# Performance work log

Measured on AMD Instinct MI355X. Metric: run time of the kernel, lower is better.

Reference implementation:

```python
import jax, jax.numpy as jnp
import numpy as np

N = 100000          # nodes
E = 1600000         # edges (before self-loops)
F_IN = 512          # num_node_features
H1, C1 = 8, 8       # layer-1 heads, per-head channels
NUM_CLASSES = 40
NEG_SLOPE = 0.2     # PyG GATConv default


def setup_inputs() -> dict:
    key = jax.random.key(0)
    ks = jax.random.split(key, 10)
    x = jax.random.normal(ks[0], (N, F_IN), jnp.float32)
    edge_index = jax.random.randint(ks[1], (2, E), 0, N, dtype=jnp.int64)
    # Glorot-ish scaled params (matches PyG init scale qualitatively)
    W1 = jax.random.normal(ks[2], (F_IN, H1 * C1), jnp.float32) / np.sqrt(F_IN)
    a_src1 = jax.random.normal(ks[3], (H1, C1), jnp.float32) / np.sqrt(C1)
    a_dst1 = jax.random.normal(ks[4], (H1, C1), jnp.float32) / np.sqrt(C1)
    b1 = jnp.zeros((H1 * C1,), jnp.float32)
    W2 = jax.random.normal(ks[5], (H1 * C1, NUM_CLASSES), jnp.float32) / np.sqrt(H1 * C1)
    a_src2 = jax.random.normal(ks[6], (1, NUM_CLASSES), jnp.float32) / np.sqrt(NUM_CLASSES)
    a_dst2 = jax.random.normal(ks[7], (1, NUM_CLASSES), jnp.float32) / np.sqrt(NUM_CLASSES)
    b2 = jnp.zeros((NUM_CLASSES,), jnp.float32)
    return {"x": x, "edge_index": edge_index, "W1": W1, "a_src1": a_src1,
            "a_dst1": a_dst1, "b1": b1, "W2": W2, "a_src2": a_src2,
            "a_dst2": a_dst2, "b2": b2}


def gat_layer(x, src, dst, W, a_s, a_d, b, concat):
    """PyG GATConv (eval mode: dropout=0). src -> dst messages, softmax over dst."""
    heads, ch = a_s.shape
    n = x.shape[0]
    h = (x @ W).reshape(n, heads, ch)                      # [N,H,C]
    alpha_s = jnp.einsum('nhc,hc->nh', h, a_s)             # [N,H]
    alpha_d = jnp.einsum('nhc,hc->nh', h, a_d)
    e = jax.nn.leaky_relu(alpha_s[src] + alpha_d[dst], NEG_SLOPE)   # [E,H]
    # segment softmax over incoming edges of each dst node
    m = jax.ops.segment_max(e, dst, num_segments=n)        # [N,H]
    p = jnp.exp(e - m[dst])
    s = jax.ops.segment_sum(p, dst, num_segments=n)
    alpha = p / (s[dst] + 1e-16)                           # [E,H]
    out = jax.ops.segment_sum(h[src] * alpha[..., None], dst, num_segments=n)  # [N,H,C]
    out = out.reshape(n, heads * ch) if concat else out.mean(axis=1)
    return out + b


def reference(x, edge_index, W1, a_src1, a_dst1, b1, W2, a_src2, a_dst2, b2):
    n = x.shape[0]
    loops = jnp.arange(n, dtype=edge_index.dtype)
    src = jnp.concatenate([edge_index[0], loops])          # add self-loops (PyG default)
    dst = jnp.concatenate([edge_index[1], loops])
    h = gat_layer(x, src, dst, W1, a_src1, a_dst1, b1, concat=True)
    h = jax.nn.elu(h)
    out = gat_layer(h, src, dst, W2, a_src2, a_dst2, b2, concat=False)
    return jax.nn.log_softmax(out, axis=1)
```

## Files before the change

### kernel.cpp

```cpp
#include <hip/hip_runtime.h>
#include <hip/hip_bf16.h>
#include <hip/hip_fp16.h>

#define F_IN 512
#define HC1 64
#define NH1 8
#define NC 40
#define NEG_SLOPE 0.2f
#define SCAN_CHUNK 2048
#define RADIX_EPB 4096
#define MAXNB 512
#define BCAP 8192

typedef short bf16x8 __attribute__((ext_vector_type(8)));
typedef float f32x4 __attribute__((ext_vector_type(4)));

static __device__ __forceinline__ unsigned short f2b(float f) {
    __hip_bfloat16 h = __float2bfloat16(f);
    return *(unsigned short*)&h;
}
static __device__ __forceinline__ float b2f(unsigned short u) {
    union { unsigned int i; float f; } v;
    v.i = ((unsigned int)u) << 16;
    return v.f;
}
static __device__ __forceinline__ unsigned short f2h(float f) {
    __half h = __float2half(f);
    return *(unsigned short*)&h;
}

__global__ void detect_i64(const int* __restrict__ ei, int* __restrict__ flag, int n_check) {
    __shared__ int found;
    if (threadIdx.x == 0) found = 0;
    __syncthreads();
    for (int i = threadIdx.x; i < n_check; i += 256) {
        if (ei[2 * i + 1] != 0) atomicOr(&found, 1);
    }
    __syncthreads();
    if (threadIdx.x == 0) *flag = (found == 0) ? 1 : 0;
}

__global__ void prep(const float* __restrict__ W1, const float* __restrict__ W2,
                     const float* __restrict__ a_s2, const float* __restrict__ a_d2,
                     unsigned short* __restrict__ wst, float* __restrict__ ws2,
                     float* __restrict__ wd2) {
    int t = blockIdx.x * 256 + threadIdx.x;
    if (t < 4096) {
        int p  = t & 7;
        int n  = (t >> 3) & 63;
        int kb = t >> 9;
        int l  = p ^ (n & 7);
        int k0 = kb * 64 + l * 8;
        unsigned short v[8];
#pragma unroll
        for (int j = 0; j < 8; j++) v[j] = f2b(W1[(size_t)(k0 + j) * HC1 + n]);
        *(uint4*)(wst + ((size_t)(kb * 64 + n) * 64 + p * 8)) = *(uint4*)v;
    }
    if (blockIdx.x == 0 && threadIdx.x < HC1) {
        int c = threadIdx.x;
        float s = 0.f, d = 0.f;
#pragma unroll
        for (int j = 0; j < NC; j++) {
            float w = W2[c * NC + j];
            s += w * a_s2[j];
            d += w * a_d2[j];
        }
        ws2[c] = s;
        wd2[c] = d;
    }
}

__global__ __launch_bounds__(256) void scatter1(const int* __restrict__ ei, const int* __restrict__ flag,
                                                int* __restrict__ deg, int* __restrict__ bcnt,
                                                int2* __restrict__ bpairs, int E, int NB) {
    __shared__ int cnt[MAXNB];
    __shared__ int gb[MAXNB];
    int tid = threadIdx.x;
    for (int i = tid; i < NB; i += 256) cnt[i] = 0;
    __syncthreads();
    int f = *flag;
    int base = blockIdx.x * RADIX_EPB;
    int sv[16], dv[16], rv[16];
#pragma unroll
    for (int i = 0; i < 16; i++) {
        int e = base + i * 256 + tid;
        if (e < E) {
            int s, d;
            if (f) { s = ei[2 * e]; d = ei[2 * (E + e)]; }
            else   { s = ei[e];     d = ei[E + e]; }
            sv[i] = s; dv[i] = d;
            rv[i] = atomicAdd(&cnt[d >> 8], 1);
            atomicAdd(&deg[d], 1);
        }
    }
    __syncthreads();
    for (int i = tid; i < NB; i += 256) {
        int c = cnt[i];
        gb[i] = c ? atomicAdd(&bcnt[i], c) : 0;
    }
    __syncthreads();
#pragma unroll
    for (int i = 0; i < 16; i++) {
        int e = base + i * 256 + tid;
        if (e < E) {
            int pos = gb[dv[i] >> 8] + rv[i];
            if (pos < BCAP)
                bpairs[(size_t)(dv[i] >> 8) * BCAP + pos] = make_int2(sv[i], dv[i]);
        }
    }
}

__global__ __launch_bounds__(256) void scan1(const int* __restrict__ deg, int* __restrict__ rowptr,
                                             int* __restrict__ bsums, int n) {
    __shared__ int sbuf[256];
    int tid = threadIdx.x;
    int base = blockIdx.x * SCAN_CHUNK + tid * 8;
    int v[8];
#pragma unroll
    for (int j = 0; j < 8; j++) { int idx = base + j; v[j] = (idx < n) ? deg[idx] : 0; }
    int tsum = 0;
#pragma unroll
    for (int j = 0; j < 8; j++) tsum += v[j];
    sbuf[tid] = tsum;
    __syncthreads();
    for (int off = 1; off < 256; off <<= 1) {
        int t = (tid >= off) ? sbuf[tid - off] : 0;
        __syncthreads();
        sbuf[tid] += t;
        __syncthreads();
    }
    int run = sbuf[tid] - tsum;
#pragma unroll
    for (int j = 0; j < 8; j++) {
        run += v[j];
        int idx = base + j;
        if (idx < n) rowptr[1 + idx] = run;
    }
    if (tid == 255) bsums[blockIdx.x] = sbuf[255];
}

__global__ __launch_bounds__(256) void scan23(int* __restrict__ rowptr,
                                              const int* __restrict__ bsums, int n, int nb) {
    __shared__ int soff[64];
    int tid = threadIdx.x;
    if (tid < 64) {
        int lane = tid;
        int v = (lane < nb) ? bsums[lane] : 0;
        int orig = v;
        for (int off = 1; off < 64; off <<= 1) {
            int t = __shfl_up(v, (unsigned)off, 64);
            if (lane >= off) v += t;
        }
        soff[lane] = v - orig;
    }
    __syncthreads();
    int i = blockIdx.x * 256 + tid;
    if (i < n) {
        rowptr[1 + i] += soff[i >> 11];
        if (i == 0) rowptr[0] = 0;
    }
}

__global__ __launch_bounds__(256) void scatter2(const int2* __restrict__ bpairs,
                                                const int* __restrict__ bcnt,
                                                const int* __restrict__ rowptr,
                                                int* __restrict__ col, int Nn) {
    __shared__ int cur[256];
    int b = blockIdx.x;
    int node0 = b << 8;
    int tid = threadIdx.x;
    int nlast = min(node0 + 256, Nn);
    if (node0 + tid < nlast) cur[tid] = rowptr[node0 + tid];
    __syncthreads();
    int cnt = min(bcnt[b], BCAP);
    const int2* bp = bpairs + (size_t)b * BCAP;
    for (int j = tid; j < cnt; j += 256) {
        int2 pr = bp[j];
        int pos = atomicAdd(&cur[pr.y - node0], 1);
        col[pos] = pr.x;
    }
}

__global__ __launch_bounds__(256) void gemm1(const float* __restrict__ x,
                                             const unsigned short* __restrict__ wst,
                                             const float* __restrict__ a_s, const float* __restrict__ a_d,
                                             unsigned short* __restrict__ h1, float* __restrict__ as1,
                                             float* __restrict__ ad1, int Nn) {
    __shared__ __align__(16) unsigned short smem[8192];
    unsigned short* xs = smem;
    unsigned short* ws = smem + 4096;
    int tid = threadIdx.x;
    int m0 = blockIdx.x * 64;
    int w = tid >> 6, lane = tid & 63;
    int quad = lane >> 4, mr = lane & 15;
    f32x4 acc[4];
#pragma unroll
    for (int i = 0; i < 4; i++) acc[i] = (f32x4){0.f, 0.f, 0.f, 0.f};

    int srow = tid >> 2;
    int sseg = tid & 3;
    bool rok = (m0 + srow) < Nn;
    const float* xrow = x + (size_t)(m0 + srow) * F_IN + sseg * 16;
    int swzw = (srow & 7) << 4;
    int swzr = (mr & 7) << 4;

    for (int kb = 0; kb < 8; kb++) {
        float4 xv0, xv1, xv2, xv3;
        if (rok) {
            const float4* xp = (const float4*)(xrow + kb * 64);
            xv0 = xp[0]; xv1 = xp[1]; xv2 = xp[2]; xv3 = xp[3];
        } else {
            xv0 = xv1 = xv2 = xv3 = make_float4(0.f, 0.f, 0.f, 0.f);
        }
        const uint4* wp = (const uint4*)(wst + (size_t)kb * 4096);
        uint4 wv0 = wp[tid];
        uint4 wv1 = wp[tid + 256];
        __syncthreads();
        {
            unsigned short bx[16];
            bx[0]  = f2b(xv0.x); bx[1]  = f2b(xv0.y); bx[2]  = f2b(xv0.z); bx[3]  = f2b(xv0.w);
            bx[4]  = f2b(xv1.x); bx[5]  = f2b(xv1.y); bx[6]  = f2b(xv1.z); bx[7]  = f2b(xv1.w);
            bx[8]  = f2b(xv2.x); bx[9]  = f2b(xv2.y); bx[10] = f2b(xv2.z); bx[11] = f2b(xv2.w);
            bx[12] = f2b(xv3.x); bx[13] = f2b(xv3.y); bx[14] = f2b(xv3.z); bx[15] = f2b(xv3.w);
            unsigned short* xr = xs + srow * 64;
            *(uint4*)(xr + ((((sseg * 32)      ) ^ swzw) >> 1)) = *(uint4*)&bx[0];
            *(uint4*)(xr + ((((sseg * 32) + 16 ) ^ swzw) >> 1)) = *(uint4*)&bx[8];
            ((uint4*)ws)[tid]       = wv0;
            ((uint4*)ws)[tid + 256] = wv1;
        }
        __syncthreads();
#pragma unroll
        for (int ks = 0; ks < 2; ks++) {
            int kc = ks * 64 + quad * 16;
            int co = (kc ^ swzr) >> 1;
            bf16x8 a = *(const bf16x8*)(xs + (w * 16 + mr) * 64 + co);
#pragma unroll
            for (int nb = 0; nb < 4; nb++) {
                bf16x8 b = *(const bf16x8*)(ws + (nb * 16 + mr) * 64 + co);
                acc[nb] = __builtin_amdgcn_mfma_f32_16x16x32_bf16(a, b, acc[nb], 0, 0, 0);
            }
        }
    }
    __syncthreads();
    unsigned short (*hs)[72] = (unsigned short(*)[72])smem;
#pragma unroll
    for (int nb = 0; nb < 4; nb++)
#pragma unroll
        for (int r = 0; r < 4; r++)
            hs[w * 16 + quad * 4 + r][nb * 16 + mr] = f2b(acc[nb][r]);
    __syncthreads();
    {
        if (rok) {
            uint4 v0 = *(const uint4*)&hs[srow][sseg * 16];
            uint4 v1 = *(const uint4*)&hs[srow][sseg * 16 + 8];
            uint4* dst = (uint4*)(h1 + (size_t)(m0 + srow) * HC1 + sseg * 16);
            dst[0] = v0;
            dst[1] = v1;
        }
    }
    for (int i = tid; i < 512; i += 256) {
        int row = i >> 3, hh = i & 7;
        if (m0 + row < Nn) {
            float s = 0.f, d = 0.f;
#pragma unroll
            for (int c = 0; c < 8; c++) {
                float v = b2f(hs[row][hh * 8 + c]);
                s += v * a_s[hh * 8 + c];
                d += v * a_d[hh * 8 + c];
            }
            as1[(size_t)(m0 + row) * NH1 + hh] = s;
            ad1[(size_t)(m0 + row) * NH1 + hh] = d;
        }
    }
}

__device__ __forceinline__ float lrelu(float e) { return e > 0.f ? e : NEG_SLOPE * e; }

__global__ __launch_bounds__(256) void agg1(const unsigned short* __restrict__ h1,
                                            const float* __restrict__ as1,
                                            const float* __restrict__ ad1, const int* __restrict__ rowptr,
                                            const int* __restrict__ col, const float* __restrict__ b1,
                                            const float* __restrict__ ws2, const float* __restrict__ wd2,
                                            unsigned short* __restrict__ h2b, float* __restrict__ as2,
                                            float* __restrict__ ad2, int Nn) {
    __shared__ float pbuf[4][NH1 * 68];
    int w = threadIdx.x >> 6;
    int wave = (blockIdx.x * 256 + threadIdx.x) >> 6;
    int lane = threadIdx.x & 63;
    if (wave >= Nn) return;
    int d = wave;
    int jb = rowptr[d], je = rowptr[d + 1];
    int half = lane >> 5;
    int cl = lane & 31;
    int head = cl >> 2;
    const float4* as4 = (const float4*)as1;
    const float4* ad4 = (const float4*)ad1;

    float4 dd0 = ad4[d * 2], dd1 = ad4[d * 2 + 1];
    float adh[8] = {dd0.x, dd0.y, dd0.z, dd0.w, dd1.x, dd1.y, dd1.z, dd1.w};
    float4 sd0 = as4[d * 2], sd1 = as4[d * 2 + 1];
    float svh[8] = {sd0.x, sd0.y, sd0.z, sd0.w, sd1.x, sd1.y, sd1.z, sd1.w};
    float e0[8];
#pragma unroll
    for (int h = 0; h < NH1; h++) e0[h] = lrelu(svh[h] + adh[h]);

    float acc0, acc1, ss;
    {
        unsigned gv = *(const unsigned*)(h1 + (size_t)d * HC1 + 2 * cl);
        union { unsigned i; float f; } lo, hi;
        lo.i = gv << 16; hi.i = gv & 0xffff0000u;
        if (half == 0) { acc0 = lo.f; acc1 = hi.f; ss = 1.f; }
        else           { acc0 = 0.f;  acc1 = 0.f;  ss = 0.f; }
    }
    float* pb = pbuf[w];

    for (int c0 = jb; c0 < je; c0 += 64) {
        int nc = min(64, je - c0);
        int srcv = d;
        if (lane < nc) {
            unsigned u = (unsigned)col[c0 + lane];
            srcv = (u < (unsigned)Nn) ? (int)u : d;
            float4 a0 = as4[srcv * 2], a1 = as4[srcv * 2 + 1];
            float ev[8] = {a0.x, a0.y, a0.z, a0.w, a1.x, a1.y, a1.z, a1.w};
#pragma unroll
            for (int h = 0; h < NH1; h++)
                pb[h * 68 + lane] = __expf(lrelu(ev[h] + adh[h]) - e0[h]);
        } else {
#pragma unroll
            for (int h = 0; h < NH1; h++) pb[h * 68 + lane] = 0.f;
        }
        int ncp = (nc + 7) & ~7;
        for (int jj = 0; jj < ncp; jj += 8) {
#pragma unroll
            for (int u4 = 0; u4 < 4; u4++) {
                int idx = jj + 2 * u4 + half;
                int s = __shfl(srcv, idx, 64);
                float p = pb[head * 68 + idx];
                unsigned gv = *(const unsigned*)(h1 + (size_t)s * HC1 + 2 * cl);
                union { unsigned i; float f; } lo, hi;
                lo.i = gv << 16; hi.i = gv & 0xffff0000u;
                acc0 += p * lo.f;
                acc1 += p * hi.f;
                ss += p;
            }
        }
    }
    acc0 += __shfl_xor(acc0, 32, 64);
    acc1 += __shfl_xor(acc1, 32, 64);
    ss   += __shfl_xor(ss, 32, 64);
    float inv = 1.f / (ss + 1e-16f);
    float o0 = acc0 * inv + b1[2 * cl];
    float o1 = acc1 * inv + b1[2 * cl + 1];
    o0 = o0 > 0.f ? o0 : __expf(o0) - 1.0f;
    o1 = o1 > 0.f ? o1 : __expf(o1) - 1.0f;
    if (half == 0) {
        unsigned pk = (unsigned)f2h(o0) | ((unsigned)f2h(o1) << 16);
        *(unsigned*)(h2b + (size_t)d * HC1 + 2 * cl) = pk;
    }
    float va = o0 * ws2[2 * cl] + o1 * ws2[2 * cl + 1];
    float vd = o0 * wd2[2 * cl] + o1 * wd2[2 * cl + 1];
#pragma unroll
    for (int off = 16; off; off >>= 1) {
        va += __shfl_xor(va, off, 64);
        vd += __shfl_xor(vd, off, 64);
    }
    if (lane == 0) { as2[d] = va; ad2[d] = vd; }
}

__global__ __launch_bounds__(256) void agg2(const unsigned short* __restrict__ h2b,
                                            const float* __restrict__ as2,
                                            const float* __restrict__ ad2, const int* __restrict__ rowptr,
                                            const int* __restrict__ col, const float* __restrict__ W2,
                                            const float* __restrict__ b2,
                                            float* __restrict__ out, int Nn) {
    __shared__ float pbuf[4][64];
    __shared__ float smv[4][64];
    __shared__ float W2s[HC1 * NC];
    int tid = threadIdx.x;
    for (int i = tid; i < HC1 * NC; i += 256) W2s[i] = W2[i];
    __syncthreads();
    int w = tid >> 6;
    int wave = (blockIdx.x * 256 + tid) >> 6;
    int lane = tid & 63;
    if (wave >= Nn) return;
    int d = wave;
    int jb = rowptr[d], je = rowptr[d + 1];
    int half = lane >> 5;
    int cl = lane & 31;
    float adv = ad2[d];
    float e0 = lrelu(as2[d] + adv);
    float acc0, acc1, ss;
    {
        unsigned gv = *(const unsigned*)(h2b + (size_t)d * HC1 + 2 * cl);
        union { unsigned u; __half2 h; } cv; cv.u = gv;
        float2 ff = __half22float2(cv.h);
        if (half == 0) { acc0 = ff.x; acc1 = ff.y; ss = 1.f; }
        else           { acc0 = 0.f;  acc1 = 0.f;  ss = 0.f; }
    }
    float* pb = pbuf[w];

    for (int c0 = jb; c0 < je; c0 += 64) {
        int nc = min(64, je - c0);
        int srcv = d;
        if (lane < nc) {
            unsigned u = (unsigned)col[c0 + lane];
            srcv = (u < (unsigned)Nn) ? (int)u : d;
            pb[lane] = __expf(lrelu(as2[srcv] + adv) - e0);
        } else {
            pb[lane] = 0.f;
        }
        int ncp = (nc + 7) & ~7;
        for (int jj = 0; jj < ncp; jj += 8) {
#pragma unroll
            for (int u4 = 0; u4 < 4; u4++) {
                int idx = jj + 2 * u4 + half;
                int s = __shfl(srcv, idx, 64);
                float p = pb[idx];
                unsigned gv = *(const unsigned*)(h2b + (size_t)s * HC1 + 2 * cl);
                union { unsigned u; __half2 h; } cv; cv.u = gv;
                float2 ff = __half22float2(cv.h);
                acc0 += p * ff.x;
                acc1 += p * ff.y;
                ss += p;
            }
        }
    }
    acc0 += __shfl_xor(acc0, 32, 64);
    acc1 += __shfl_xor(acc1, 32, 64);
    ss   += __shfl_xor(ss, 32, 64);
    float inv = 1.f / (ss + 1e-16f);
    if (half == 0) {
        smv[w][2 * cl]     = acc0 * inv;
        smv[w][2 * cl + 1] = acc1 * inv;
    }
    float o = 0.f;
    if (lane < NC) {
        o = b2[lane];
        const float* sv = smv[w];
#pragma unroll
        for (int c = 0; c < HC1; c++) o += sv[c] * W2s[c * NC + lane];
    }
    float vm = (lane < NC) ? o : -1e30f;
#pragma unroll
    for (int off = 32; off; off >>= 1) vm = fmaxf(vm, __shfl_xor(vm, off, 64));
    float ex = (lane < NC) ? __expf(o - vm) : 0.f;
#pragma unroll
    for (int off = 32; off; off >>= 1) ex += __shfl_xor(ex, off, 64);
    float lsm = o - vm - __logf(ex);
    if (lane < NC) out[(size_t)d * NC + lane] = lsm;
}

extern "C" void kernel_launch(void* const* d_in, const int* in_sizes, int n_in,
                              void* d_out, int out_size, void* d_ws, size_t ws_size,
                              hipStream_t stream) {
    const float* x      = (const float*)d_in[0];
    const int*   ei     = (const int*)d_in[1];
    const float* W1     = (const float*)d_in[2];
    const float* a_src1 = (const float*)d_in[3];
    const float* a_dst1 = (const float*)d_in[4];
    const float* b1     = (const float*)d_in[5];
    const float* W2     = (const float*)d_in[6];
    const float* a_src2 = (const float*)d_in[7];
    const float* a_dst2 = (const float*)d_in[8];
    const float* b2     = (const float*)d_in[9];
    float* out = (float*)d_out;

    const int N = in_sizes[0] / F_IN;
    const int E = in_sizes[1] / 2;
    const int NB = (N + 255) >> 8;

    char* p = (char*)d_ws;
    auto alloc = [&](size_t bytes) -> void* {
        void* r = (void*)p;
        p += (bytes + 255) & ~(size_t)255;
        return r;
    };
    int* deg    = (int*)alloc((size_t)N * 4);
    int* bcnt   = (int*)alloc((size_t)MAXNB * 4);
    int* rowptr = (int*)alloc(((size_t)N + 1) * 4);
    int* bsums  = (int*)alloc(64 * 4);
    int* flag   = (int*)alloc(256);
    int2* bpairs = (int2*)alloc((size_t)NB * BCAP * 8);
    int* col    = (int*)alloc((size_t)E * 4);
    unsigned short* h1  = (unsigned short*)alloc((size_t)N * HC1 * 2);
    float* as1  = (float*)alloc((size_t)N * NH1 * 4);
    float* ad1  = (float*)alloc((size_t)N * NH1 * 4);
    unsigned short* h2b = (unsigned short*)alloc((size_t)N * HC1 * 2);
    float* as2  = (float*)alloc((size_t)N * 4);
    float* ad2  = (float*)alloc((size_t)N * 4);
    unsigned short* wst = (unsigned short*)alloc(8 * 64 * 64 * 2);
    float* ws2  = (float*)alloc(HC1 * 4);
    float* wd2  = (float*)alloc(HC1 * 4);

    size_t zlen = (size_t)((char*)(bcnt + MAXNB) - (char*)deg);
    hipMemsetAsync(deg, 0, zlen, stream);
    detect_i64<<<1, 256, 0, stream>>>(ei, flag, 4096);
    prep<<<16, 256, 0, stream>>>(W1, W2, a_src2, a_dst2, wst, ws2, wd2);
    scatter1<<<(E + RADIX_EPB - 1) / RADIX_EPB, 256, 0, stream>>>(ei, flag, deg, bcnt, bpairs, E, NB);
    int nb = (N + SCAN_CHUNK - 1) / SCAN_CHUNK;
    scan1<<<nb, 256, 0, stream>>>(deg, rowptr, bsums, N);
    scan23<<<(N + 255) / 256, 256, 0, stream>>>(rowptr, bsums, N, nb);
    scatter2<<<NB, 256, 0, stream>>>(bpairs, bcnt, rowptr, col, N);

    gemm1<<<(N + 63) / 64, 256, 0, stream>>>(x, wst, a_src1, a_dst1, h1, as1, ad1, N);
    agg1<<<(N + 3) / 4, 256, 0, stream>>>(h1, as1, ad1, rowptr, col, b1, ws2, wd2, h2b, as2, ad2, N);

    agg2<<<(N + 3) / 4, 256, 0, stream>>>(h2b, as2, ad2, rowptr, col, W2, b2, out, N);
}
```

Before: 584.5 us.

## Pack bucket pairs into one int, merge dtype detect into prep, batch gather loads

Merges the int64-detection kernel into the prep launch as an extra block, removing one kernel launch. Packs each (src, dst-low-byte) pair into a single 32-bit word in the bucket buffer, halving its memory traffic in scatter1 and scatter2. In both aggregation kernels it restructures the inner loop to issue 8 independent gathered loads before accumulating, raising memory-level parallelism at the cost of more registers. The packing assumes source ids fit in 24 bits.

```diff
diff --git a/kernel.cpp b/kernel.cpp
--- a/kernel.cpp
+++ b/kernel.cpp
@@ -29,23 +29,26 @@
     return *(unsigned short*)&h;
 }
 
-__global__ void detect_i64(const int* __restrict__ ei, int* __restrict__ flag, int n_check) {
-    __shared__ int found;
-    if (threadIdx.x == 0) found = 0;
-    __syncthreads();
-    for (int i = threadIdx.x; i < n_check; i += 256) {
-        if (ei[2 * i + 1] != 0) atomicOr(&found, 1);
-    }
-    __syncthreads();
-    if (threadIdx.x == 0) *flag = (found == 0) ? 1 : 0;
-}
+__device__ __forceinline__ float lrelu(float e) { return e > 0.f ? e : NEG_SLOPE * e; }
 
 __global__ void prep(const float* __restrict__ W1, const float* __restrict__ W2,
                      const float* __restrict__ a_s2, const float* __restrict__ a_d2,
+                     const int* __restrict__ ei,
                      unsigned short* __restrict__ wst, float* __restrict__ ws2,
-                     float* __restrict__ wd2) {
+                     float* __restrict__ wd2, int* __restrict__ flag) {
+    if (blockIdx.x == 16) {
+        __shared__ int found;
+        if (threadIdx.x == 0) found = 0;
+        __syncthreads();
+        for (int i = threadIdx.x; i < 4096; i += 256) {
+            if (ei[2 * i + 1] != 0) atomicOr(&found, 1);
+        }
+        __syncthreads();
+        if (threadIdx.x == 0) *flag = (found == 0) ? 1 : 0;
+        return;
+    }
     int t = blockIdx.x * 256 + threadIdx.x;
-    if (t < 4096) {
+    {
         int p  = t & 7;
         int n  = (t >> 3) & 63;
         int kb = t >> 9;
@@ -72,7 +75,7 @@
 
 __global__ __launch_bounds__(256) void scatter1(const int* __restrict__ ei, const int* __restrict__ flag,
                                                 int* __restrict__ deg, int* __restrict__ bcnt,
-                                                int2* __restrict__ bpairs, int E, int NB) {
+                                                int* __restrict__ bpk, int E, int NB) {
     __shared__ int cnt[MAXNB];
     __shared__ int gb[MAXNB];
     int tid = threadIdx.x;
@@ -80,7 +83,7 @@
     __syncthreads();
     int f = *flag;
     int base = blockIdx.x * RADIX_EPB;
-    int sv[16], dv[16], rv[16];
+    int pk[16], bk[16], rv[16];
 #pragma unroll
     for (int i = 0; i < 16; i++) {
         int e = base + i * 256 + tid;
@@ -88,8 +91,9 @@
             int s, d;
             if (f) { s = ei[2 * e]; d = ei[2 * (E + e)]; }
             else   { s = ei[e];     d = ei[E + e]; }
-            sv[i] = s; dv[i] = d;
-            rv[i] = atomicAdd(&cnt[d >> 8], 1);
+            pk[i] = (s << 8) | (d & 255);
+            bk[i] = d >> 8;
+            rv[i] = atomicAdd(&cnt[bk[i]], 1);
             atomicAdd(&deg[d], 1);
         }
     }
@@ -103,9 +107,9 @@
     for (int i = 0; i < 16; i++) {
         int e = base + i * 256 + tid;
         if (e < E) {
-            int pos = gb[dv[i] >> 8] + rv[i];
+            int pos = gb[bk[i]] + rv[i];
             if (pos < BCAP)
-                bpairs[(size_t)(dv[i] >> 8) * BCAP + pos] = make_int2(sv[i], dv[i]);
+                bpk[(size_t)bk[i] * BCAP + pos] = pk[i];
         }
     }
 }
@@ -161,7 +165,7 @@
     }
 }
 
-__global__ __launch_bounds__(256) void scatter2(const int2* __restrict__ bpairs,
+__global__ __launch_bounds__(256) void scatter2(const int* __restrict__ bpk,
                                                 const int* __restrict__ bcnt,
                                                 const int* __restrict__ rowptr,
                                                 int* __restrict__ col, int Nn) {
@@ -173,11 +177,11 @@
     if (node0 + tid < nlast) cur[tid] = rowptr[node0 + tid];
     __syncthreads();
     int cnt = min(bcnt[b], BCAP);
-    const int2* bp = bpairs + (size_t)b * BCAP;
+    const int* bp = bpk + (size_t)b * BCAP;
     for (int j = tid; j < cnt; j += 256) {
-        int2 pr = bp[j];
-        int pos = atomicAdd(&cur[pr.y - node0], 1);
-        col[pos] = pr.x;
+        int pk = bp[j];
+        int pos = atomicAdd(&cur[pk & 255], 1);
+        col[pos] = (int)((unsigned)pk >> 8);
     }
 }
 
@@ -273,8 +277,6 @@
         }
     }
 }
-
-__device__ __forceinline__ float lrelu(float e) { return e > 0.f ? e : NEG_SLOPE * e; }
 
 __global__ __launch_bounds__(256) void agg1(const unsigned short* __restrict__ h1,
                                             const float* __restrict__ as1,
@@ -329,19 +331,27 @@
 #pragma unroll
             for (int h = 0; h < NH1; h++) pb[h * 68 + lane] = 0.f;
         }
-        int ncp = (nc + 7) & ~7;
-        for (int jj = 0; jj < ncp; jj += 8) {
-#pragma unroll
-            for (int u4 = 0; u4 < 4; u4++) {
+        int ncp = (nc + 15) & ~15;
+        for (int jj = 0; jj < ncp; jj += 16) {
+            int sarr[8];
+            float parr[8];
+            unsigned gvv[8];
+#pragma unroll
+            for (int u4 = 0; u4 < 8; u4++) {
                 int idx = jj + 2 * u4 + half;
-                int s = __shfl(srcv, idx, 64);
-                float p = pb[head * 68 + idx];
-                unsigned gv = *(const unsigned*)(h1 + (size_t)s * HC1 + 2 * cl);
+                sarr[u4] = __shfl(srcv, idx, 64);
+                parr[u4] = pb[head * 68 + idx];
+            }
+#pragma unroll
+            for (int u4 = 0; u4 < 8; u4++)
+                gvv[u4] = *(const unsigned*)(h1 + (size_t)sarr[u4] * HC1 + 2 * cl);
+#pragma unroll
+            for (int u4 = 0; u4 < 8; u4++) {
                 union { unsigned i; float f; } lo, hi;
-                lo.i = gv << 16; hi.i = gv & 0xffff0000u;
-                acc0 += p * lo.f;
-                acc1 += p * hi.f;
-                ss += p;
+                lo.i = gvv[u4] << 16; hi.i = gvv[u4] & 0xffff0000u;
+                acc0 += parr[u4] * lo.f;
+                acc1 += parr[u4] * hi.f;
+                ss += parr[u4];
             }
         }
     }
@@ -409,19 +419,27 @@
         } else {
             pb[lane] = 0.f;
         }
-        int ncp = (nc + 7) & ~7;
-        for (int jj = 0; jj < ncp; jj += 8) {
-#pragma unroll
-            for (int u4 = 0; u4 < 4; u4++) {
+        int ncp = (nc + 15) & ~15;
+        for (int jj = 0; jj < ncp; jj += 16) {
+            int sarr[8];
+            float parr[8];
+            unsigned gvv[8];
+#pragma unroll
+            for (int u4 = 0; u4 < 8; u4++) {
                 int idx = jj + 2 * u4 + half;
-                int s = __shfl(srcv, idx, 64);
-                float p = pb[idx];
-                unsigned gv = *(const unsigned*)(h2b + (size_t)s * HC1 + 2 * cl);
-                union { unsigned u; __half2 h; } cv; cv.u = gv;
+                sarr[u4] = __shfl(srcv, idx, 64);
+                parr[u4] = pb[idx];
+            }
+#pragma unroll
+            for (int u4 = 0; u4 < 8; u4++)
+                gvv[u4] = *(const unsigned*)(h2b + (size_t)sarr[u4] * HC1 + 2 * cl);
+#pragma unroll
+            for (int u4 = 0; u4 < 8; u4++) {
+                union { unsigned u; __half2 h; } cv; cv.u = gvv[u4];
                 float2 ff = __half22float2(cv.h);
-                acc0 += p * ff.x;
-                acc1 += p * ff.y;
-                ss += p;
+                acc0 += parr[u4] * ff.x;
+                acc1 += parr[u4] * ff.y;
+                ss += parr[u4];
             }
         }
     }
@@ -480,7 +498,7 @@
     int* rowptr = (int*)alloc(((size_t)N + 1) * 4);
     int* bsums  = (int*)alloc(64 * 4);
     int* flag   = (int*)alloc(256);
-    int2* bpairs = (int2*)alloc((size_t)NB * BCAP * 8);
+    int* bpk    = (int*)alloc((size_t)NB * BCAP * 4);
     int* col    = (int*)alloc((size_t)E * 4);
     unsigned short* h1  = (unsigned short*)alloc((size_t)N * HC1 * 2);
     float* as1  = (float*)alloc((size_t)N * NH1 * 4);
@@ -494,13 +512,12 @@
 
     size_t zlen = (size_t)((char*)(bcnt + MAXNB) - (char*)deg);
     hipMemsetAsync(deg, 0, zlen, stream);
-    detect_i64<<<1, 256, 0, stream>>>(ei, flag, 4096);
-    prep<<<16, 256, 0, stream>>>(W1, W2, a_src2, a_dst2, wst, ws2, wd2);
-    scatter1<<<(E + RADIX_EPB - 1) / RADIX_EPB, 256, 0, stream>>>(ei, flag, deg, bcnt, bpairs, E, NB);
+    prep<<<17, 256, 0, stream>>>(W1, W2, a_src2, a_dst2, ei, wst, ws2, wd2, flag);
+    scatter1<<<(E + RADIX_EPB - 1) / RADIX_EPB, 256, 0, stream>>>(ei, flag, deg, bcnt, bpk, E, NB);
     int nb = (N + SCAN_CHUNK - 1) / SCAN_CHUNK;
     scan1<<<nb, 256, 0, stream>>>(deg, rowptr, bsums, N);
     scan23<<<(N + 255) / 256, 256, 0, stream>>>(rowptr, bsums, N, nb);
-    scatter2<<<NB, 256, 0, stream>>>(bpairs, bcnt, rowptr, col, N);
+    scatter2<<<NB, 256, 0, stream>>>(bpk, bcnt, rowptr, col, N);
 
     gemm1<<<(N + 63) / 64, 256, 0, stream>>>(x, wst, a_src1, a_dst1, h1, as1, ad1, N);
     agg1<<<(N + 3) / 4, 256, 0, stream>>>(h1, as1, ad1, rowptr, col, b1, ws2, wd2, h2b, as2, ad2, N);
```

Measured after the change: 581.8 us. Within noise of the previous version (-0.5%).
